# Kernel optimization log

Hardware: AMD Instinct MI355X
Metric: run time of the kernel (lower is better)

The kernel has to match this reference:

```python
import jax, jax.numpy as jnp
import numpy as np

V, H, HP, HOUT, G = 500_000, 128, 128, 128, 25_000


def setup_inputs() -> dict:
    key = jax.random.key(0)
    ks = jax.random.split(key, 7)
    node_features = jax.random.normal(ks[0], (V, H), dtype=jnp.float32)
    s = jnp.float32(1.0 / np.sqrt(H))
    W_up = jax.random.normal(ks[1], (H, HP), dtype=jnp.float32) * s
    b_up = jax.random.normal(ks[2], (HP,), dtype=jnp.float32) * jnp.float32(0.02)
    W_gate = jax.random.normal(ks[3], (H, HP), dtype=jnp.float32) * s
    b_gate = jax.random.normal(ks[4], (HP,), dtype=jnp.float32) * jnp.float32(0.02)
    W_func = jax.random.normal(ks[5], (HP, HOUT), dtype=jnp.float32) * s
    b_func = jax.random.normal(ks[6], (HOUT,), dtype=jnp.float32) * jnp.float32(0.02)
    # graph offsets: G graphs, each with >=2 nodes, summing exactly to V (sorted, last = V)
    rng = np.random.default_rng(0)
    sizes = rng.multinomial(V - 2 * G, np.full(G, 1.0 / G)) + 2
    starts = np.concatenate([[0], np.cumsum(sizes)]).astype(np.int64)
    assert starts[-1] == V
    node_grp_start_with_end = jnp.asarray(starts)
    max_size = int(sizes.max())
    return {
        "node_features": node_features,
        "W_up": W_up, "b_up": b_up,
        "W_gate": W_gate, "b_gate": b_gate,
        "W_func": W_func, "b_func": b_func,
        "node_grp_start_with_end": node_grp_start_with_end,
        "max_size": max_size,
    }


def reference(node_features, W_up, b_up, W_gate, b_gate, W_func, b_func,
              node_grp_start_with_end, max_size):
    starts = node_grp_start_with_end  # [g+1], sorted, starts[-1] == v
    g = starts.shape[0] - 1
    v = node_features.shape[0]

    proj_up = node_features @ W_up + b_up            # [v, hp]
    gate = jax.nn.sigmoid(node_features @ W_gate + b_gate)
    gated = gate * proj_up                            # [v, hp]

    # segment id of each node: graph i where starts[i] <= n < starts[i+1]
    n = jnp.arange(v)
    seg = jnp.searchsorted(starts, n, side="right") - 1  # [v]

    # faithful to original loop: end = next_start - 1, so the LAST node of each
    # graph is EXCLUDED from the padded copy (and hence from the sum)
    keep = n != (starts[seg + 1] - 1)                 # [v] bool

    graph_sums = jax.ops.segment_sum(
        jnp.where(keep[:, None], gated, jnp.float32(0.0)), seg, num_segments=g
    )                                                 # [g, hp]

    return graph_sums @ W_func + b_func               # [g, h_out]
```

## Files before the change

### kernel.cpp

```cpp
#include <hip/hip_runtime.h>


typedef __bf16 bf16_t;
typedef bf16_t bf16x8 __attribute__((ext_vector_type(8)));
typedef float  f32x4  __attribute__((ext_vector_type(4)));

#define XS_STRIDE 144

__device__ __forceinline__ unsigned short f2bf(float f) {
  unsigned int u = __float_as_uint(f);
  u += 0x7fffu + ((u >> 16) & 1u);
  return (unsigned short)(u >> 16);
}

__device__ __forceinline__ void bar_lds() {
  asm volatile("s_waitcnt lgkmcnt(0)\n\ts_barrier" ::: "memory");
}

__global__ void tile_seg_kernel(const int* __restrict__ starts,
                                int* __restrict__ tile_seg,
                                int ntiles, int G) {
  int i = blockIdx.x * blockDim.x + threadIdx.x;
  if (i >= ntiles) return;
  int n0 = i * 64;
  int lo = 0, hi = G - 1;
  while (lo < hi) {
    int mid = (lo + hi + 1) >> 1;
    if (starts[mid] <= n0) lo = mid; else hi = mid - 1;
  }
  tile_seg[i] = lo;
}

__global__ __launch_bounds__(256, 2)
void stage1_kernel(const float* __restrict__ X,
                   const float* __restrict__ Wu, const float* __restrict__ bu,
                   const float* __restrict__ Wg, const float* __restrict__ bg,
                   const int* __restrict__ starts,
                   const int* __restrict__ tile_seg,
                   float* __restrict__ gsum, int V, int G, int ntiles)
{
  __shared__ unsigned short Xs[2][64 * XS_STRIDE];

  const int tid  = threadIdx.x;
  const int lane = tid & 63;
  const int wave = tid >> 6;
  const int quad = lane >> 4;
  const int l15  = lane & 15;

  bf16x8 Bu[2][4], Bg[2][4];
  float bup[2], bgt[2];
#pragma unroll
  for (int t = 0; t < 2; ++t) {
    const int f = wave * 32 + t * 16 + l15;
    bup[t] = bu[f];
    bgt[t] = bg[f];
#pragma unroll
    for (int s = 0; s < 4; ++s) {
      const int k0 = s * 32 + quad * 8;
      union { unsigned short us[8]; bf16x8 v; } a, b;
#pragma unroll
      for (int j = 0; j < 8; ++j) {
        a.us[j] = f2bf(Wu[(k0 + j) * 128 + f]);
        b.us[j] = f2bf(Wg[(k0 + j) * 128 + f]);
      }
      Bu[t][s] = a.v;
      Bg[t][s] = b.v;
    }
  }

  f32x4 ld[8];
  int tile = blockIdx.x;

  int g0v, sval;
  {
    const int t0 = min(tile, ntiles - 1);
    g0v  = tile_seg[t0];
    sval = starts[min(g0v + lane, G)];
    const int n0 = t0 * 64;
#pragma unroll
    for (int i = 0; i < 8; ++i) {
      const int flat = tid + i * 256;
      const int n = min(n0 + (flat >> 5), V - 1);
      const int k = (flat & 31) << 2;
      ld[i] = *(const f32x4*)(X + (size_t)n * 128 + k);
    }
  }

  int it = 0;
  for (; tile < ntiles; tile += gridDim.x, ++it) {
    const int n0    = tile * 64;
    const int n_end = min(n0 + 64, V);
    const int g0 = g0v;
    const int sv = sval;
    unsigned short* xb = Xs[it & 1];

#pragma unroll
    for (int i = 0; i < 8; ++i) {
      const int flat = tid + i * 256;
      const int n = flat >> 5;
      const int k = (flat & 31) << 2;
      const unsigned int p0 =
          (unsigned int)f2bf(ld[i][0]) | ((unsigned int)f2bf(ld[i][1]) << 16);
      const unsigned int p1 =
          (unsigned int)f2bf(ld[i][2]) | ((unsigned int)f2bf(ld[i][3]) << 16);
      *(uint2*)&xb[n * XS_STRIDE + k] = make_uint2(p0, p1);
    }

    const int nextc = min(tile + (int)gridDim.x, ntiles - 1);
    {
      const int m0 = nextc * 64;
#pragma unroll
      for (int i = 0; i < 8; ++i) {
        const int flat = tid + i * 256;
        const int n = min(m0 + (flat >> 5), V - 1);
        const int k = (flat & 31) << 2;
        ld[i] = *(const f32x4*)(X + (size_t)n * 128 + k);
      }
    }
    g0v  = tile_seg[nextc];
    sval = starts[min(g0v + lane, G)];

    bar_lds();

    float gv[4][2][4];
#pragma unroll
    for (int sub = 0; sub < 4; ++sub) {
      bf16x8 A[4];
      const int nl = sub * 16 + l15;
#pragma unroll
      for (int s = 0; s < 4; ++s)
        A[s] = *(const bf16x8*)&xb[nl * XS_STRIDE + s * 32 + quad * 8];
#pragma unroll
      for (int t = 0; t < 2; ++t) {
        f32x4 au = {0.f, 0.f, 0.f, 0.f};
        f32x4 ag = {0.f, 0.f, 0.f, 0.f};
#pragma unroll
        for (int s = 0; s < 4; ++s) {
          au = __builtin_amdgcn_mfma_f32_16x16x32_bf16(A[s], Bu[t][s], au, 0, 0, 0);
          ag = __builtin_amdgcn_mfma_f32_16x16x32_bf16(A[s], Bg[t][s], ag, 0, 0, 0);
        }
#pragma unroll
        for (int r = 0; r < 4; ++r) {
          const float up = au[r] + bup[t];
          const float gt = ag[r] + bgt[t];
          gv[sub][t][r] = up * __builtin_amdgcn_rcpf(1.f + __expf(-gt));
        }
      }
    }

    {
      int i = 0;
      int sg = __shfl(sv, 0);
      while (sg < n_end && i < 63) {
        const int snext = __shfl(sv, i + 1);
        const int r0 = max(sg, n0) - n0;
        const int r1 = min(snext - 1, n_end) - n0;
        if (r1 > r0) {
          float p0 = 0.f, p1 = 0.f;
#pragma unroll
          for (int sub = 0; sub < 4; ++sub) {
#pragma unroll
            for (int r = 0; r < 4; ++r) {
              const int row = sub * 16 + quad * 4 + r;
              const bool in = (row >= r0) && (row < r1);
              p0 += in ? gv[sub][0][r] : 0.f;
              p1 += in ? gv[sub][1][r] : 0.f;
            }
          }
          p0 += __shfl_xor(p0, 16); p0 += __shfl_xor(p0, 32);
          p1 += __shfl_xor(p1, 16); p1 += __shfl_xor(p1, 32);
          if (quad == 0)
            atomicAdd(&gsum[(size_t)(g0 + i) * 128 + wave * 32 + l15], p0);
          else if (quad == 1)
            atomicAdd(&gsum[(size_t)(g0 + i) * 128 + wave * 32 + 16 + l15], p1);
        }
        sg = snext;
        ++i;
      }
    }
  }
}

__global__ __launch_bounds__(256)
void stage2_kernel(const float* __restrict__ Wf, const float* __restrict__ bfv,
                   float* __restrict__ out, int G)
{
  __shared__ float Gsm[32 * 132];
  const int g0  = blockIdx.x * 32;
  const int tid = threadIdx.x;

  for (int i = tid; i < 32 * 32; i += 256) {
    const int r = i >> 5;
    const int c = (i & 31) << 2;
    const int g = g0 + r;
    f32x4 v = {0.f, 0.f, 0.f, 0.f};
    if (g < G) v = *(const f32x4*)(out + (size_t)g * 128 + c);
    *(f32x4*)&Gsm[r * 132 + c] = v;
  }
  __syncthreads();

  const int fq  = tid & 31;
  const int f0  = fq << 2;
  const int grp = tid >> 5;
  float acc[4][4];
#pragma unroll
  for (int i = 0; i < 4; ++i)
#pragma unroll
    for (int j = 0; j < 4; ++j) acc[i][j] = 0.f;

#pragma unroll 4
  for (int k = 0; k < 128; ++k) {
    const f32x4 w = *(const f32x4*)(Wf + (size_t)k * 128 + f0);
#pragma unroll
    for (int i = 0; i < 4; ++i) {
      const float gv = Gsm[(grp * 4 + i) * 132 + k];
      acc[i][0] += gv * w[0];
      acc[i][1] += gv * w[1];
      acc[i][2] += gv * w[2];
      acc[i][3] += gv * w[3];
    }
  }

  const f32x4 bb = *(const f32x4*)(bfv + f0);
#pragma unroll
  for (int i = 0; i < 4; ++i) {
    const int g = g0 + grp * 4 + i;
    if (g < G) {
      f32x4 o = {acc[i][0] + bb[0], acc[i][1] + bb[1],
                 acc[i][2] + bb[2], acc[i][3] + bb[3]};
      *(f32x4*)(out + (size_t)g * 128 + f0) = o;
    }
  }
}

extern "C" void kernel_launch(void* const* d_in, const int* in_sizes, int n_in,
                              void* d_out, int out_size, void* d_ws, size_t ws_size,
                              hipStream_t stream)
{
  const float* X      = (const float*)d_in[0];
  const float* Wu     = (const float*)d_in[1];
  const float* bu     = (const float*)d_in[2];
  const float* Wg     = (const float*)d_in[3];
  const float* bg     = (const float*)d_in[4];
  const float* Wf     = (const float*)d_in[5];
  const float* bf_    = (const float*)d_in[6];
  const int*   starts = (const int*)d_in[7];

  const int G = in_sizes[7] - 1;
  const int V = in_sizes[0] / 128;
  const int ntiles = (V + 63) / 64;

  int*   tile_seg = (int*)d_ws;
  float* gsum     = (float*)d_out;

  hipMemsetAsync(d_out, 0, (size_t)G * 128 * sizeof(float), stream);
  tile_seg_kernel<<<(ntiles + 255) / 256, 256, 0, stream>>>(starts, tile_seg, ntiles, G);
  stage1_kernel<<<512, 256, 0, stream>>>(X, Wu, bu, Wg, bg, starts, tile_seg,
                                         gsum, V, G, ntiles);
  stage2_kernel<<<(G + 31) / 32, 256, 0, stream>>>(Wf, bf_, gsum, G);
}
```

Before: 399.1 us.

## Partition stage1 by graph groups with LDS accumulation instead of global atomics

Stage1 now assigns each block a fixed group of 50 graphs and walks only that group's node range, accumulating per-graph sums in shared memory before writing them out once. This removes the memset, the tile-segment binary-search kernel, and the global float atomics. In exchange the grid grows to about 500 short-lived blocks that each reload and convert the weights into registers, and the per-block tile count varies with graph sizes. Tiles no longer align to 64-node boundaries across blocks, and the LDS footprint grows, which may limit occupancy.

```diff
diff --git a/kernel.cpp b/kernel.cpp
--- a/kernel.cpp
+++ b/kernel.cpp
@@ -6,6 +6,7 @@
 typedef float  f32x4  __attribute__((ext_vector_type(4)));
 
 #define XS_STRIDE 144
+#define GPB 50
 
 __device__ __forceinline__ unsigned short f2bf(float f) {
   unsigned int u = __float_as_uint(f);
@@ -15,20 +16,6 @@
 
 __device__ __forceinline__ void bar_lds() {
   asm volatile("s_waitcnt lgkmcnt(0)\n\ts_barrier" ::: "memory");
-}
-
-__global__ void tile_seg_kernel(const int* __restrict__ starts,
-                                int* __restrict__ tile_seg,
-                                int ntiles, int G) {
-  int i = blockIdx.x * blockDim.x + threadIdx.x;
-  if (i >= ntiles) return;
-  int n0 = i * 64;
-  int lo = 0, hi = G - 1;
-  while (lo < hi) {
-    int mid = (lo + hi + 1) >> 1;
-    if (starts[mid] <= n0) lo = mid; else hi = mid - 1;
-  }
-  tile_seg[i] = lo;
 }
 
 __global__ __launch_bounds__(256, 2)
@@ -36,10 +23,10 @@
                    const float* __restrict__ Wu, const float* __restrict__ bu,
                    const float* __restrict__ Wg, const float* __restrict__ bg,
                    const int* __restrict__ starts,
-                   const int* __restrict__ tile_seg,
-                   float* __restrict__ gsum, int V, int G, int ntiles)
+                   float* __restrict__ gsum, int V, int G)
 {
   __shared__ unsigned short Xs[2][64 * XS_STRIDE];
+  __shared__ float          acc[GPB * 128];
 
   const int tid  = threadIdx.x;
   const int lane = tid & 63;
@@ -47,6 +34,14 @@
   const int quad = lane >> 4;
   const int l15  = lane & 15;
 
+  const int g_lo = blockIdx.x * GPB;
+  const int ng   = min(GPB, G - g_lo);
+  if (ng <= 0) return;
+
+  const int sv      = starts[min(g_lo + lane, G)];
+  const int node_lo = __shfl(sv, 0);
+  const int node_hi = __shfl(sv, ng);
+
   bf16x8 Bu[2][4], Bg[2][4];
   float bup[2], bgt[2];
 #pragma unroll
@@ -68,31 +63,25 @@
     }
   }
 
+  for (int i = tid; i < GPB * 32; i += 256)
+    *(f32x4*)&acc[i << 2] = f32x4{0.f, 0.f, 0.f, 0.f};
+
+  const int ntl = (node_hi - node_lo + 63) >> 6;
+
   f32x4 ld[8];
-  int tile = blockIdx.x;
-
-  int g0v, sval;
-  {
-    const int t0 = min(tile, ntiles - 1);
-    g0v  = tile_seg[t0];
-    sval = starts[min(g0v + lane, G)];
-    const int n0 = t0 * 64;
-#pragma unroll
-    for (int i = 0; i < 8; ++i) {
-      const int flat = tid + i * 256;
-      const int n = min(n0 + (flat >> 5), V - 1);
-      const int k = (flat & 31) << 2;
-      ld[i] = *(const f32x4*)(X + (size_t)n * 128 + k);
-    }
-  }
-
-  int it = 0;
-  for (; tile < ntiles; tile += gridDim.x, ++it) {
-    const int n0    = tile * 64;
-    const int n_end = min(n0 + 64, V);
-    const int g0 = g0v;
-    const int sv = sval;
-    unsigned short* xb = Xs[it & 1];
+#pragma unroll
+  for (int i = 0; i < 8; ++i) {
+    const int flat = tid + i * 256;
+    const int n = min(node_lo + (flat >> 5), V - 1);
+    const int k = (flat & 31) << 2;
+    ld[i] = *(const f32x4*)(X + (size_t)n * 128 + k);
+  }
+
+  int gi = 0;
+  for (int t = 0; t < ntl; ++t) {
+    unsigned short* xb = Xs[t & 1];
+    const int n0g   = node_lo + t * 64;
+    const int n_end = min(n0g + 64, node_hi);
 
 #pragma unroll
     for (int i = 0; i < 8; ++i) {
@@ -106,9 +95,8 @@
       *(uint2*)&xb[n * XS_STRIDE + k] = make_uint2(p0, p1);
     }
 
-    const int nextc = min(tile + (int)gridDim.x, ntiles - 1);
     {
-      const int m0 = nextc * 64;
+      const int m0 = node_lo + min(t + 1, ntl - 1) * 64;
 #pragma unroll
       for (int i = 0; i < 8; ++i) {
         const int flat = tid + i * 256;
@@ -117,8 +105,6 @@
         ld[i] = *(const f32x4*)(X + (size_t)n * 128 + k);
       }
     }
-    g0v  = tile_seg[nextc];
-    sval = starts[min(g0v + lane, G)];
 
     bar_lds();
 
@@ -131,30 +117,30 @@
       for (int s = 0; s < 4; ++s)
         A[s] = *(const bf16x8*)&xb[nl * XS_STRIDE + s * 32 + quad * 8];
 #pragma unroll
-      for (int t = 0; t < 2; ++t) {
+      for (int tt = 0; tt < 2; ++tt) {
         f32x4 au = {0.f, 0.f, 0.f, 0.f};
         f32x4 ag = {0.f, 0.f, 0.f, 0.f};
 #pragma unroll
         for (int s = 0; s < 4; ++s) {
-          au = __builtin_amdgcn_mfma_f32_16x16x32_bf16(A[s], Bu[t][s], au, 0, 0, 0);
-          ag = __builtin_amdgcn_mfma_f32_16x16x32_bf16(A[s], Bg[t][s], ag, 0, 0, 0);
+          au = __builtin_amdgcn_mfma_f32_16x16x32_bf16(A[s], Bu[tt][s], au, 0, 0, 0);
+          ag = __builtin_amdgcn_mfma_f32_16x16x32_bf16(A[s], Bg[tt][s], ag, 0, 0, 0);
         }
 #pragma unroll
         for (int r = 0; r < 4; ++r) {
-          const float up = au[r] + bup[t];
-          const float gt = ag[r] + bgt[t];
-          gv[sub][t][r] = up * __builtin_amdgcn_rcpf(1.f + __expf(-gt));
+          const float up = au[r] + bup[tt];
+          const float gt = ag[r] + bgt[tt];
+          gv[sub][tt][r] = up * __builtin_amdgcn_rcpf(1.f + __expf(-gt));
         }
       }
     }
 
     {
-      int i = 0;
-      int sg = __shfl(sv, 0);
-      while (sg < n_end && i < 63) {
+      int i = gi;
+      int sg = __shfl(sv, i);
+      while (i < ng && sg < n_end) {
         const int snext = __shfl(sv, i + 1);
-        const int r0 = max(sg, n0) - n0;
-        const int r1 = min(snext - 1, n_end) - n0;
+        const int r0 = max(sg, n0g) - n0g;
+        const int r1 = min(snext - 1, n_end) - n0g;
         if (r1 > r0) {
           float p0 = 0.f, p1 = 0.f;
 #pragma unroll
@@ -170,14 +156,23 @@
           p0 += __shfl_xor(p0, 16); p0 += __shfl_xor(p0, 32);
           p1 += __shfl_xor(p1, 16); p1 += __shfl_xor(p1, 32);
           if (quad == 0)
-            atomicAdd(&gsum[(size_t)(g0 + i) * 128 + wave * 32 + l15], p0);
+            acc[i * 128 + wave * 32 + l15] += p0;
           else if (quad == 1)
-            atomicAdd(&gsum[(size_t)(g0 + i) * 128 + wave * 32 + 16 + l15], p1);
+            acc[i * 128 + wave * 32 + 16 + l15] += p1;
         }
+        if (snext > n_end) break;
         sg = snext;
         ++i;
       }
-    }
+      gi = i;
+    }
+  }
+
+  __syncthreads();
+  for (int i = tid; i < ng * 32; i += 256) {
+    const int row = i >> 5;
+    const int c   = (i & 31) << 2;
+    *(f32x4*)(gsum + (size_t)(g_lo + row) * 128 + c) = *(const f32x4*)&acc[row * 128 + c];
   }
 }
 
@@ -202,11 +197,11 @@
   const int fq  = tid & 31;
   const int f0  = fq << 2;
   const int grp = tid >> 5;
-  float acc[4][4];
+  float acc2[4][4];
 #pragma unroll
   for (int i = 0; i < 4; ++i)
 #pragma unroll
-    for (int j = 0; j < 4; ++j) acc[i][j] = 0.f;
+    for (int j = 0; j < 4; ++j) acc2[i][j] = 0.f;
 
 #pragma unroll 4
   for (int k = 0; k < 128; ++k) {
@@ -214,10 +209,10 @@
 #pragma unroll
     for (int i = 0; i < 4; ++i) {
       const float gv = Gsm[(grp * 4 + i) * 132 + k];
-      acc[i][0] += gv * w[0];
-      acc[i][1] += gv * w[1];
-      acc[i][2] += gv * w[2];
-      acc[i][3] += gv * w[3];
+      acc2[i][0] += gv * w[0];
+      acc2[i][1] += gv * w[1];
+      acc2[i][2] += gv * w[2];
+      acc2[i][3] += gv * w[3];
     }
   }
 
@@ -226,8 +221,8 @@
   for (int i = 0; i < 4; ++i) {
     const int g = g0 + grp * 4 + i;
     if (g < G) {
-      f32x4 o = {acc[i][0] + bb[0], acc[i][1] + bb[1],
-                 acc[i][2] + bb[2], acc[i][3] + bb[3]};
+      f32x4 o = {acc2[i][0] + bb[0], acc2[i][1] + bb[1],
+                 acc2[i][2] + bb[2], acc2[i][3] + bb[3]};
       *(f32x4*)(out + (size_t)g * 128 + f0) = o;
     }
   }
@@ -248,14 +243,10 @@
 
   const int G = in_sizes[7] - 1;
   const int V = in_sizes[0] / 128;
-  const int ntiles = (V + 63) / 64;
-
-  int*   tile_seg = (int*)d_ws;
-  float* gsum     = (float*)d_out;
-
-  hipMemsetAsync(d_out, 0, (size_t)G * 128 * sizeof(float), stream);
-  tile_seg_kernel<<<(ntiles + 255) / 256, 256, 0, stream>>>(starts, tile_seg, ntiles, G);
-  stage1_kernel<<<512, 256, 0, stream>>>(X, Wu, bu, Wg, bg, starts, tile_seg,
-                                         gsum, V, G, ntiles);
+
+  float* gsum = (float*)d_out;
+  const int nb1 = (G + GPB - 1) / GPB;
+
+  stage1_kernel<<<nb1, 256, 0, stream>>>(X, Wu, bu, Wg, bg, starts, gsum, V, G);
   stage2_kernel<<<(G + 31) / 32, 256, 0, stream>>>(Wf, bf_, gsum, G);
 }
```

Result: no change. 403.3 us (+1.0%).
